# Kernel tuning notes

Hardware: AMD Instinct MI355X
Metric: run time of the kernel (lower is better)

## Reference

```python
import jax, jax.numpy as jnp
import numpy as np

B, S, H = 32, 4096, 512


def setup_inputs() -> dict:
    key = jax.random.key(0)
    ks = jax.random.split(key, 6)
    return {
        "tree_inputs": jax.random.normal(ks[0], (B, H), dtype=jnp.float32),
        "tree_context": jax.random.normal(ks[1], (S, B, H), dtype=jnp.float32),
        "text_inputs": jax.random.normal(ks[2], (B, H), dtype=jnp.float32),
        "text_context": jax.random.normal(ks[3], (S, B, H), dtype=jnp.float32),
        "tree_mask": jnp.ones((B, S), dtype=jnp.float32),
        "text_mask": jnp.ones((B, S), dtype=jnp.float32),
        "W_in": jax.random.normal(ks[4], (H, H), dtype=jnp.float32) * (1.0 / np.sqrt(H)),
        "W_out": jax.random.normal(ks[5], (4 * H, H), dtype=jnp.float32) * (1.0 / np.sqrt(4 * H)),
    }


def _branch(inputs, context_sbh, mask, W_in):
    # context arrives [S,B,H]; original code uses tf.reshape (NOT transpose) to [B,S,H]
    s, b, h = context_sbh.shape
    ctx = context_sbh.reshape(b, s, h)  # faithful reshape semantics
    target = inputs @ W_in  # [B,H]
    scores = jnp.einsum('bsh,bh->bs', ctx, target)  # masked-matmul scores
    scores = scores * mask  # inline mask-multiply before softmax (as in original)
    att = jax.nn.softmax(scores, axis=-1)  # [B,S]
    weighted = jnp.einsum('bs,bsh->bh', att, ctx)  # context-weighting
    return att, weighted


def reference(tree_inputs, tree_context, text_inputs, text_context,
              tree_mask, text_mask, W_in, W_out):
    tree_att, tree_w = _branch(tree_inputs, tree_context, tree_mask, W_in)
    text_att, text_w = _branch(text_inputs, text_context, text_mask, W_in)
    combined = jnp.concatenate([tree_w, tree_inputs, text_w, text_inputs], axis=1)  # [B,4H]
    combined = jnp.tanh(combined @ W_out)  # fused linear_out + tanh, [B,H]
    return combined, tree_att, text_att
```

## Files before the change

### kernel.cpp

```cpp
#include <hip/hip_runtime.h>
#include <math.h>

#define BB 32
#define SS 4096
#define HH 512
#define CHUNKS 32
#define ROWS_PER_BLOCK 128
#define ROWS_PER_WAVE 32
#define TROWS 2
#define NTILES (ROWS_PER_WAVE / TROWS)

#define WS_TPART    0
#define WS_SCORES   262144
#define WS_PML      524288
#define WS_PACC     528384
#define WS_WEIGHTED 1576960
#define WS_GPART    1609728

__device__ static inline void gload_lds16(const float* g, float* l) {
    __builtin_amdgcn_global_load_lds(
        (const __attribute__((address_space(1))) void*)g,
        (__attribute__((address_space(3))) void*)l, 16, 0, 0);
}
__device__ static inline void gload_lds16_nt(const float* g, float* l) {
    __builtin_amdgcn_global_load_lds(
        (const __attribute__((address_space(1))) void*)g,
        (__attribute__((address_space(3))) void*)l, 16, 0, 2 );
}

__global__ __launch_bounds__(256) void k_target(
    const float* __restrict__ tree_in, const float* __restrict__ text_in,
    const float* __restrict__ W_in, float* __restrict__ ws)
{
    const int rc = blockIdx.x;
    const int bb = blockIdx.y;
    const int br = bb >> 5, b = bb & 31;
    const float* inp = (br == 0 ? tree_in : text_in) + b * HH;

    __shared__ float sx[64];
    if (threadIdx.x < 64) sx[threadIdx.x] = inp[rc * 64 + threadIdx.x];
    __syncthreads();

    const int c = threadIdx.x;
    const float* wp = W_in + (size_t)(rc * 64) * HH + c;
    float a0 = 0.f, a1 = 0.f;
    #pragma unroll 8
    for (int j = 0; j < 64; ++j) {
        const float x = sx[j];
        a0 += x * wp[(size_t)j * HH];
        a1 += x * wp[(size_t)j * HH + 256];
    }
    float* tp = ws + WS_TPART + (size_t)(rc * 64 + bb) * HH;
    tp[c] = a0;
    tp[c + 256] = a1;
}

__global__ __launch_bounds__(256) void k_flash(
    const float* __restrict__ tree_ctx, const float* __restrict__ text_ctx,
    const float* __restrict__ tree_mask, const float* __restrict__ text_mask,
    float* __restrict__ ws)
{
    const int br = blockIdx.x;
    const int chunk = blockIdx.y;
    const int b = blockIdx.z;
    const int bi = br * BB + b;

    const float* ctx = (br == 0 ? tree_ctx : text_ctx) + (size_t)b * SS * HH;
    const float* mask = (br == 0 ? tree_mask : text_mask) + (size_t)b * SS;
    float* scores_g = ws + WS_SCORES + (size_t)bi * SS;

    const int wave = threadIdx.x >> 6;
    const int lane = threadIdx.x & 63;
    const int lane4 = lane * 4;

    __shared__ float smem[4 * 2 * 1024 + 128 + 128 + 8 + 8];
    float* const tiles_w = smem + wave * 2048;
    float* const smask = smem + 8192;
    float* const ssc = smem + 8320;
    float* const lm = smem + 8448;
    float* const ll = smem + 8456;

    float* const buf0 = tiles_w;
    float* const buf1 = tiles_w + 1024;
    const int s0 = chunk * ROWS_PER_BLOCK + wave * ROWS_PER_WAVE;
    const int r0 = wave * ROWS_PER_WAVE;

    #define ISSUE_TILE(TT, BP) do {                                          \
        const float* _g = ctx + (size_t)(s0 + (TT) * TROWS) * HH + lane4;    \
        if (br == 0) {                                                       \
            _Pragma("unroll")                                                \
            for (int j = 0; j < 4; ++j)                                      \
                gload_lds16(_g + j * 256, (BP) + j * 256);                   \
        } else {                                                             \
            _Pragma("unroll")                                                \
            for (int j = 0; j < 4; ++j)                                      \
                gload_lds16_nt(_g + j * 256, (BP) + j * 256);                \
        }                                                                    \
    } while (0)

    ISSUE_TILE(0, buf0);
    __builtin_amdgcn_sched_barrier(0);

    if (threadIdx.x < ROWS_PER_BLOCK)
        smask[threadIdx.x] = mask[chunk * ROWS_PER_BLOCK + threadIdx.x];

    float4 t0 = make_float4(0.f, 0.f, 0.f, 0.f);
    float4 t1 = make_float4(0.f, 0.f, 0.f, 0.f);
    #pragma unroll
    for (int rc = 0; rc < 8; ++rc) {
        const float* tp = ws + WS_TPART + (size_t)(rc * 64 + bi) * HH;
        const float4 u = *(const float4*)(tp + lane4);
        const float4 v = *(const float4*)(tp + 256 + lane4);
        t0.x += u.x; t0.y += u.y; t0.z += u.z; t0.w += u.w;
        t1.x += v.x; t1.y += v.y; t1.z += v.z; t1.w += v.w;
    }
    __syncthreads();

    float m = -INFINITY, l = 0.f;
    float4 acc_a = make_float4(0.f, 0.f, 0.f, 0.f);
    float4 acc_b = make_float4(0.f, 0.f, 0.f, 0.f);

    for (int tt = 0; tt < NTILES; ++tt) {
        if (tt + 1 < NTILES) {
            float* nb = ((tt + 1) & 1) ? buf1 : buf0;
            ISSUE_TILE(tt + 1, nb);
            asm volatile("s_waitcnt vmcnt(4)" ::: "memory");
        } else {
            asm volatile("s_waitcnt vmcnt(0)" ::: "memory");
        }
        __builtin_amdgcn_sched_barrier(0);

        const float* bp = (tt & 1) ? buf1 : buf0;
        const int rbase = r0 + tt * TROWS;

        const float4 c00 = *(const float4*)(bp + lane4);
        const float4 c01 = *(const float4*)(bp + 256 + lane4);
        const float4 c10 = *(const float4*)(bp + 512 + lane4);
        const float4 c11 = *(const float4*)(bp + 768 + lane4);

        float d0 = c00.x*t0.x + c00.y*t0.y + c00.z*t0.z + c00.w*t0.w
                 + c01.x*t1.x + c01.y*t1.y + c01.z*t1.z + c01.w*t1.w;
        float d1 = c10.x*t0.x + c10.y*t0.y + c10.z*t0.z + c10.w*t0.w
                 + c11.x*t1.x + c11.y*t1.y + c11.z*t1.z + c11.w*t1.w;
        #pragma unroll
        for (int off = 1; off < 64; off <<= 1) {
            d0 += __shfl_xor(d0, off);
            d1 += __shfl_xor(d1, off);
        }

        const float sc0 = d0 * smask[rbase + 0];
        const float sc1 = d1 * smask[rbase + 1];
        if (lane == 0) ssc[rbase + 0] = sc0;
        if (lane == 1) ssc[rbase + 1] = sc1;

        const float mx = fmaxf(sc0, sc1);
        if (mx > m + 8.f) {
            const float e = __expf(m - mx);
            l *= e;
            acc_a.x *= e; acc_a.y *= e; acc_a.z *= e; acc_a.w *= e;
            acc_b.x *= e; acc_b.y *= e; acc_b.z *= e; acc_b.w *= e;
            m = mx;
        }
        const float p0 = __expf(sc0 - m);
        const float p1 = __expf(sc1 - m);
        l += p0 + p1;

        acc_a.x += p0*c00.x + p1*c10.x;
        acc_a.y += p0*c00.y + p1*c10.y;
        acc_a.z += p0*c00.z + p1*c10.z;
        acc_a.w += p0*c00.w + p1*c10.w;
        acc_b.x += p0*c01.x + p1*c11.x;
        acc_b.y += p0*c01.y + p1*c11.y;
        acc_b.z += p0*c01.z + p1*c11.z;
        acc_b.w += p0*c01.w + p1*c11.w;
    }
    #undef ISSUE_TILE

    __syncthreads();
    float* const lacc_w = tiles_w;
    if (lane == 0) { lm[wave] = m; ll[wave] = l; }
    *(float4*)(lacc_w + lane4) = acc_a;
    *(float4*)(lacc_w + 256 + lane4) = acc_b;
    __syncthreads();

    const float M = fmaxf(fmaxf(lm[0], lm[1]), fmaxf(lm[2], lm[3]));
    const float e0 = __expf(lm[0] - M);
    const float e1 = __expf(lm[1] - M);
    const float e2 = __expf(lm[2] - M);
    const float e3 = __expf(lm[3] - M);

    float* pml = ws + WS_PML + (size_t)(bi * CHUNKS + chunk) * 2;
    float* pacc = ws + WS_PACC + (size_t)(bi * CHUNKS + chunk) * HH;
    for (int h = threadIdx.x; h < HH; h += 256)
        pacc[h] = smem[0 * 2048 + h] * e0 + smem[1 * 2048 + h] * e1
                + smem[2 * 2048 + h] * e2 + smem[3 * 2048 + h] * e3;
    if (threadIdx.x == 0) {
        pml[0] = M;
        pml[1] = ll[0] * e0 + ll[1] * e1 + ll[2] * e2 + ll[3] * e3;
    }
    if (threadIdx.x < ROWS_PER_BLOCK)
        scores_g[chunk * ROWS_PER_BLOCK + threadIdx.x] = ssc[threadIdx.x];
}

__global__ __launch_bounds__(256) void k_merge(
    const float* __restrict__ ws_ro, float* __restrict__ ws, float* __restrict__ out)
{
    const int br = blockIdx.x;
    const int b = blockIdx.y;
    const int hs = blockIdx.z;
    const int bi = br * BB + b;
    const int tid = threadIdx.x;

    const float* pml = ws_ro + WS_PML + (size_t)bi * CHUNKS * 2;
    __shared__ float esc[CHUNKS];
    float M = -INFINITY;
    for (int c = 0; c < CHUNKS; ++c) M = fmaxf(M, pml[2 * c]);
    float L = 0.f;
    for (int c = 0; c < CHUNKS; ++c) L += pml[2 * c + 1] * __expf(pml[2 * c] - M);
    const float invL = 1.f / L;
    if (tid < CHUNKS) esc[tid] = __expf(pml[2 * tid] - M) * invL;
    __syncthreads();

    const float* pacc = ws_ro + WS_PACC + (size_t)bi * CHUNKS * HH;
    float* wt = ws + WS_WEIGHTED + (size_t)bi * HH;
    if (tid < 128) {
        const int h = hs * 128 + tid;
        float a = 0.f;
        for (int c = 0; c < CHUNKS; ++c) a += pacc[(size_t)c * HH + h] * esc[c];
        wt[h] = a;
    }

    const float* sc_g = ws_ro + WS_SCORES + (size_t)bi * SS;
    float* att = out + BB * HH + (size_t)bi * SS;
    {
        const int s4 = hs * 1024 + tid * 4;
        const float4 sc = *(const float4*)(sc_g + s4);
        float4 r;
        r.x = __expf(sc.x - M) * invL;
        r.y = __expf(sc.y - M) * invL;
        r.z = __expf(sc.z - M) * invL;
        r.w = __expf(sc.w - M) * invL;
        *(float4*)(att + s4) = r;
    }
}

__global__ __launch_bounds__(256) void k_gemv(
    const float* __restrict__ tree_in, const float* __restrict__ text_in,
    const float* __restrict__ W_out, const float* __restrict__ ws_ro,
    float* __restrict__ ws)
{
    const int rc = blockIdx.x;
    const int half = blockIdx.y;
    const int b = blockIdx.z;
    const int tid = threadIdx.x;

    const int seg = rc >> 2;
    const float* src;
    if (seg == 0)      src = ws_ro + WS_WEIGHTED + (size_t)(0 * BB + b) * HH;
    else if (seg == 1) src = tree_in + (size_t)b * HH;
    else if (seg == 2) src = ws_ro + WS_WEIGHTED + (size_t)(1 * BB + b) * HH;
    else               src = text_in + (size_t)b * HH;

    __shared__ float sx[128];
    if (tid < 128) sx[tid] = src[(rc & 3) * 128 + tid];
    __syncthreads();

    const float* wp = W_out + (size_t)(rc * 128) * HH + half * 256 + tid;
    float a = 0.f;
    #pragma unroll 8
    for (int j = 0; j < 128; ++j)
        a += sx[j] * wp[(size_t)j * HH];

    ws[WS_GPART + (size_t)((rc * 2 + half) * BB + b) * 256 + tid] = a;
}

__global__ __launch_bounds__(256) void k_fin(
    const float* __restrict__ ws, float* __restrict__ out)
{
    const int half = blockIdx.x;
    const int b = blockIdx.y;
    const int tid = threadIdx.x;
    float v = 0.f;
    #pragma unroll
    for (int rc = 0; rc < 16; ++rc)
        v += ws[WS_GPART + (size_t)((rc * 2 + half) * BB + b) * 256 + tid];
    out[(size_t)b * HH + half * 256 + tid] = tanhf(v);
}

extern "C" void kernel_launch(void* const* d_in, const int* in_sizes, int n_in,
                              void* d_out, int out_size, void* d_ws, size_t ws_size,
                              hipStream_t stream)
{
    const float* tree_inputs  = (const float*)d_in[0];
    const float* tree_context = (const float*)d_in[1];
    const float* text_inputs  = (const float*)d_in[2];
    const float* text_context = (const float*)d_in[3];
    const float* tree_mask    = (const float*)d_in[4];
    const float* text_mask    = (const float*)d_in[5];
    const float* W_in         = (const float*)d_in[6];
    const float* W_out        = (const float*)d_in[7];
    float* out = (float*)d_out;
    float* ws = (float*)d_ws;

    k_target<<<dim3(8, 64), 256, 0, stream>>>(tree_inputs, text_inputs, W_in, ws);
    k_flash<<<dim3(2, CHUNKS, BB), 256, 0, stream>>>(tree_context, text_context,
                                                     tree_mask, text_mask, ws);
    k_merge<<<dim3(2, BB, 4), 256, 0, stream>>>(ws, ws, out);
    k_gemv<<<dim3(16, 2, BB), 256, 0, stream>>>(tree_inputs, text_inputs, W_out, ws, ws);
    k_fin<<<dim3(2, BB), 256, 0, stream>>>(ws, out);
}
```

Before: 112.8 us.

## Fuse merge into W_out GEMV and hoist input-only GEMV into head kernel

The GEMV over the raw tree/text inputs against W_out no longer depends on attention, so it moves into the first kernel alongside the W_in target projection. The merge step, which rescales chunk partials and writes attention probabilities, is fused with the GEMV over the weighted context, so the weighted vectors stay in shared memory instead of going through the workspace. This drops one launch and one global round trip. In exchange, each fused block redundantly recomputes the per-row max and sum from the chunk partials.

New measurement: 114.8 us. No clear change (+1.7%).

```diff
diff --git a/kernel.cpp b/kernel.cpp
--- a/kernel.cpp
+++ b/kernel.cpp
@@ -14,7 +14,6 @@
 #define WS_SCORES   262144
 #define WS_PML      524288
 #define WS_PACC     528384
-#define WS_WEIGHTED 1576960
 #define WS_GPART    1609728
 
 __device__ static inline void gload_lds16(const float* g, float* l) {
@@ -28,31 +27,57 @@
         (__attribute__((address_space(3))) void*)l, 16, 0, 2 );
 }
 
-__global__ __launch_bounds__(256) void k_target(
+__global__ __launch_bounds__(256) void k_head(
     const float* __restrict__ tree_in, const float* __restrict__ text_in,
-    const float* __restrict__ W_in, float* __restrict__ ws)
-{
-    const int rc = blockIdx.x;
-    const int bb = blockIdx.y;
-    const int br = bb >> 5, b = bb & 31;
-    const float* inp = (br == 0 ? tree_in : text_in) + b * HH;
-
-    __shared__ float sx[64];
-    if (threadIdx.x < 64) sx[threadIdx.x] = inp[rc * 64 + threadIdx.x];
-    __syncthreads();
-
-    const int c = threadIdx.x;
-    const float* wp = W_in + (size_t)(rc * 64) * HH + c;
-    float a0 = 0.f, a1 = 0.f;
-    #pragma unroll 8
-    for (int j = 0; j < 64; ++j) {
-        const float x = sx[j];
-        a0 += x * wp[(size_t)j * HH];
-        a1 += x * wp[(size_t)j * HH + 256];
-    }
-    float* tp = ws + WS_TPART + (size_t)(rc * 64 + bb) * HH;
-    tp[c] = a0;
-    tp[c + 256] = a1;
+    const float* __restrict__ W_in, const float* __restrict__ W_out,
+    float* __restrict__ ws)
+{
+    const int x = blockIdx.x;
+    const int y = blockIdx.y;
+    const int tid = threadIdx.x;
+    __shared__ float sx[128];
+
+    if (y < 64) {
+        const int rc = x;
+        const int bb = y;
+        const int br = bb >> 5, b = bb & 31;
+        const float* inp = (br == 0 ? tree_in : text_in) + b * HH;
+
+        if (tid < 64) sx[tid] = inp[rc * 64 + tid];
+        __syncthreads();
+
+        const float* wp = W_in + (size_t)(rc * 64) * HH + tid;
+        float a0 = 0.f, a1 = 0.f;
+        #pragma unroll 8
+        for (int j = 0; j < 64; ++j) {
+            const float xx = sx[j];
+            a0 += xx * wp[(size_t)j * HH];
+            a1 += xx * wp[(size_t)j * HH + 256];
+        }
+        float* tp = ws + WS_TPART + (size_t)(rc * 64 + bb) * HH;
+        tp[tid] = a0;
+        tp[tid + 256] = a1;
+    } else {
+        const int rcp = x;
+        const int half = (y - 64) >> 5;
+        const int b = (y - 64) & 31;
+        const int seg = (rcp < 4) ? 1 : 3;
+        const int slice = rcp & 3;
+        const int gi = seg * 4 + slice;
+        const float* src = (seg == 1 ? tree_in : text_in) + (size_t)b * HH;
+
+        if (tid < 128) sx[tid] = src[slice * 128 + tid];
+        __syncthreads();
+
+        const float* wp = W_out + (size_t)(seg * 512 + slice * 128) * HH
+                        + half * 256 + tid;
+        float a = 0.f;
+        #pragma unroll 8
+        for (int j = 0; j < 128; ++j)
+            a += sx[j] * wp[(size_t)j * HH];
+
+        ws[WS_GPART + (size_t)((gi * 2 + half) * BB + b) * 256 + tid] = a;
+    }
 }
 
 __global__ __launch_bounds__(256) void k_flash(
@@ -202,17 +227,24 @@
         scores_g[chunk * ROWS_PER_BLOCK + threadIdx.x] = ssc[threadIdx.x];
 }
 
-__global__ __launch_bounds__(256) void k_merge(
-    const float* __restrict__ ws_ro, float* __restrict__ ws, float* __restrict__ out)
-{
-    const int br = blockIdx.x;
-    const int b = blockIdx.y;
-    const int hs = blockIdx.z;
+__global__ __launch_bounds__(256) void k_wgemv(
+    const float* __restrict__ W_out, const float* __restrict__ ws_ro,
+    float* __restrict__ ws, float* __restrict__ out)
+{
+    const int rcp = blockIdx.x;
+    const int half = blockIdx.y;
+    const int b = blockIdx.z;
+    const int tid = threadIdx.x;
+
+    const int br = (rcp < 4) ? 0 : 1;
+    const int wseg = br * 2;
+    const int slice = rcp & 3;
+    const int gi = wseg * 4 + slice;
     const int bi = br * BB + b;
-    const int tid = threadIdx.x;
 
     const float* pml = ws_ro + WS_PML + (size_t)bi * CHUNKS * 2;
     __shared__ float esc[CHUNKS];
+    __shared__ float sw[128];
     float M = -INFINITY;
     for (int c = 0; c < CHUNKS; ++c) M = fmaxf(M, pml[2 * c]);
     float L = 0.f;
@@ -222,56 +254,33 @@
     __syncthreads();
 
     const float* pacc = ws_ro + WS_PACC + (size_t)bi * CHUNKS * HH;
-    float* wt = ws + WS_WEIGHTED + (size_t)bi * HH;
     if (tid < 128) {
-        const int h = hs * 128 + tid;
+        const int h = slice * 128 + tid;
         float a = 0.f;
         for (int c = 0; c < CHUNKS; ++c) a += pacc[(size_t)c * HH + h] * esc[c];
-        wt[h] = a;
-    }
-
-    const float* sc_g = ws_ro + WS_SCORES + (size_t)bi * SS;
-    float* att = out + BB * HH + (size_t)bi * SS;
+        sw[tid] = a;
+    }
+
     {
-        const int s4 = hs * 1024 + tid * 4;
-        const float4 sc = *(const float4*)(sc_g + s4);
-        float4 r;
+        const float* sc_g = ws_ro + WS_SCORES + (size_t)bi * SS;
+        float* att = out + BB * HH + (size_t)bi * SS;
+        const int s2 = (slice * 2 + half) * 512 + tid * 2;
+        const float2 sc = *(const float2*)(sc_g + s2);
+        float2 r;
         r.x = __expf(sc.x - M) * invL;
         r.y = __expf(sc.y - M) * invL;
-        r.z = __expf(sc.z - M) * invL;
-        r.w = __expf(sc.w - M) * invL;
-        *(float4*)(att + s4) = r;
-    }
-}
-
-__global__ __launch_bounds__(256) void k_gemv(
-    const float* __restrict__ tree_in, const float* __restrict__ text_in,
-    const float* __restrict__ W_out, const float* __restrict__ ws_ro,
-    float* __restrict__ ws)
-{
-    const int rc = blockIdx.x;
-    const int half = blockIdx.y;
-    const int b = blockIdx.z;
-    const int tid = threadIdx.x;
-
-    const int seg = rc >> 2;
-    const float* src;
-    if (seg == 0)      src = ws_ro + WS_WEIGHTED + (size_t)(0 * BB + b) * HH;
-    else if (seg == 1) src = tree_in + (size_t)b * HH;
-    else if (seg == 2) src = ws_ro + WS_WEIGHTED + (size_t)(1 * BB + b) * HH;
-    else               src = text_in + (size_t)b * HH;
-
-    __shared__ float sx[128];
-    if (tid < 128) sx[tid] = src[(rc & 3) * 128 + tid];
-    __syncthreads();
-
-    const float* wp = W_out + (size_t)(rc * 128) * HH + half * 256 + tid;
+        *(float2*)(att + s2) = r;
+    }
+    __syncthreads();
+
+    const float* wp = W_out + (size_t)(wseg * 512 + slice * 128) * HH
+                    + half * 256 + tid;
     float a = 0.f;
     #pragma unroll 8
     for (int j = 0; j < 128; ++j)
-        a += sx[j] * wp[(size_t)j * HH];
-
-    ws[WS_GPART + (size_t)((rc * 2 + half) * BB + b) * 256 + tid] = a;
+        a += sw[j] * wp[(size_t)j * HH];
+
+    ws[WS_GPART + (size_t)((gi * 2 + half) * BB + b) * 256 + tid] = a;
 }
 
 __global__ __launch_bounds__(256) void k_fin(
@@ -282,8 +291,8 @@
     const int tid = threadIdx.x;
     float v = 0.f;
     #pragma unroll
-    for (int rc = 0; rc < 16; ++rc)
-        v += ws[WS_GPART + (size_t)((rc * 2 + half) * BB + b) * 256 + tid];
+    for (int gi = 0; gi < 16; ++gi)
+        v += ws[WS_GPART + (size_t)((gi * 2 + half) * BB + b) * 256 + tid];
     out[(size_t)b * HH + half * 256 + tid] = tanhf(v);
 }
 
@@ -302,10 +311,10 @@
     float* out = (float*)d_out;
     float* ws = (float*)d_ws;
 
-    k_target<<<dim3(8, 64), 256, 0, stream>>>(tree_inputs, text_inputs, W_in, ws);
+    k_head<<<dim3(8, 128), 256, 0, stream>>>(tree_inputs, text_inputs,
+                                             W_in, W_out, ws);
     k_flash<<<dim3(2, CHUNKS, BB), 256, 0, stream>>>(tree_context, text_context,
                                                      tree_mask, text_mask, ws);
-    k_merge<<<dim3(2, BB, 4), 256, 0, stream>>>(ws, ws, out);
-    k_gemv<<<dim3(16, 2, BB), 256, 0, stream>>>(tree_inputs, text_inputs, W_out, ws, ws);
+    k_wgemv<<<dim3(8, 2, BB), 256, 0, stream>>>(W_out, ws, ws, out);
     k_fin<<<dim3(2, BB), 256, 0, stream>>>(ws, out);
 }
```
